# Kernel tuning notes

Hardware: AMD Instinct MI355X
Metric: run time of the kernel (lower is better)

## Reference

```python
import jax, jax.numpy as jnp
import numpy as np

OUTPUT_DIM = 1024  # init kwarg output_dim


def _adaptive_avg_pool_last(x, out_dim):
    """Faithful F.adaptive_avg_pool1d over the last axis (static shapes)."""
    in_dim = x.shape[-1]
    if in_dim % out_dim == 0:
        k = in_dim // out_dim
        return x.reshape(x.shape[:-1] + (out_dim, k)).mean(axis=-1)
    # generic case: window i covers [floor(i*In/Out), ceil((i+1)*In/Out))
    idx = np.arange(out_dim)
    starts = (idx * in_dim) // out_dim
    ends = -((-(idx + 1) * in_dim) // out_dim)
    W = np.zeros((in_dim, out_dim), dtype=np.float32)
    for i in range(out_dim):
        W[starts[i]:ends[i], i] = 1.0 / (ends[i] - starts[i])
    return x @ jnp.asarray(W)


def _per_layer_gram(feat, output_dim):
    N, C, ph, pw = feat.shape
    P = ph * pw
    c_red = min(C, 64)
    f = feat.reshape(N, C, P).transpose(0, 2, 1)        # [N, P, C]
    f = _adaptive_avg_pool_last(f, c_red)               # [N, P, Cr] channel reduction
    fr = f.transpose(0, 2, 1)                           # [N, Cr, P]
    gram = jnp.einsum('ncp,ndp->ncd', fr, fr) / P       # [N, Cr, Cr] per-patch Gram
    return _adaptive_avg_pool_last(gram.reshape(N, c_red * c_red), output_dim)  # [N, output_dim]


def setup_inputs() -> dict:
    key = jax.random.key(0)
    k0, k1 = jax.random.split(key)
    feat0 = jax.random.normal(k0, (6272, 512, 3, 3), dtype=jnp.float32)
    feat1 = jax.random.normal(k1, (6272, 1024, 3, 3), dtype=jnp.float32)
    return {"feat0": feat0, "feat1": feat1}


def reference(feat0, feat1):
    # stack over layers -> [N, L=2, output_dim]
    return jnp.stack(
        [_per_layer_gram(feat0, OUTPUT_DIM), _per_layer_gram(feat1, OUTPUT_DIM)],
        axis=1,
    )
```

## Files before the change

### kernel.cpp

```cpp
#include <hip/hip_runtime.h>


#define N_SAMPLES 6272

template <int CH>
__global__ __launch_bounds__(CH / 4) void patchgram_reg(
    const float* __restrict__ src, float* __restrict__ out)
{
    constexpr int T   = CH / 4;
    constexpr int K   = CH / 64;
    constexpr int TPR = K / 4;
    constexpr float SCALE = 1.0f / (36.0f * (float)(K * K));

    __shared__ float4 fr4[64 * 3];
    __shared__ float4 B4[16 * 3];

    const int n = blockIdx.x;
    const int t = threadIdx.x;

    const float4* __restrict__ g =
        (const float4*)(src + (size_t)n * (CH * 9)) + t * 9;

    float acc[9];
#pragma unroll
    for (int p = 0; p < 9; ++p) acc[p] = 0.f;
#pragma unroll
    for (int j = 0; j < 9; ++j) {
        const float4 v = g[j];
        acc[(4 * j + 0) % 9] += v.x;
        acc[(4 * j + 1) % 9] += v.y;
        acc[(4 * j + 2) % 9] += v.z;
        acc[(4 * j + 3) % 9] += v.w;
    }

#pragma unroll
    for (int p = 0; p < 9; ++p) acc[p] += __shfl_xor(acc[p], 1);
    if (TPR == 4) {
#pragma unroll
        for (int p = 0; p < 9; ++p) acc[p] += __shfl_xor(acc[p], 2);
    }
    if ((t & (TPR - 1)) == 0) {
        const int row = t / TPR;
        fr4[row * 3 + 0] = make_float4(acc[0], acc[1], acc[2], acc[3]);
        fr4[row * 3 + 1] = make_float4(acc[4], acc[5], acc[6], acc[7]);
        fr4[row * 3 + 2] = make_float4(acc[8], 0.f, 0.f, 0.f);
    }
    __syncthreads();

    for (int i = t; i < 144; i += T) {
        const int dg = i / 9;
        const int p  = i - dg * 9;
        const float* fr = (const float*)fr4;
        ((float*)B4)[dg * 12 + p] =
            fr[(4 * dg + 0) * 12 + p] + fr[(4 * dg + 1) * 12 + p] +
            fr[(4 * dg + 2) * 12 + p] + fr[(4 * dg + 3) * 12 + p];
    }
    __syncthreads();

    constexpr int OPT = 1024 / T;
    constexpr int GPR = 16 / OPT;
    const int c     = t / GPR;
    const int dbase = (t % GPR) * OPT;

    const float4 a0 = fr4[c * 3 + 0];
    const float4 a1 = fr4[c * 3 + 1];
    const float4 a2 = fr4[c * 3 + 2];

    float o[OPT];
#pragma unroll
    for (int j = 0; j < OPT; ++j) {
        const int d = dbase + j;
        const float4 b0 = B4[d * 3 + 0];
        const float4 b1 = B4[d * 3 + 1];
        const float4 b2 = B4[d * 3 + 2];
        o[j] = (a0.x * b0.x + a0.y * b0.y + a0.z * b0.z + a0.w * b0.w
              + a1.x * b1.x + a1.y * b1.y + a1.z * b1.z + a1.w * b1.w
              + a2.x * b2.x) * SCALE;
    }

    float* obase = out + (size_t)n * 2048 + c * 16 + dbase;
#pragma unroll
    for (int q = 0; q < OPT / 4; ++q) {
        ((float4*)obase)[q] =
            make_float4(o[4 * q + 0], o[4 * q + 1], o[4 * q + 2], o[4 * q + 3]);
    }
}

extern "C" void kernel_launch(void* const* d_in, const int* in_sizes, int n_in,
                              void* d_out, int out_size, void* d_ws, size_t ws_size,
                              hipStream_t stream) {
    const float* f0 = (const float*)d_in[0];
    const float* f1 = (const float*)d_in[1];
    float* out = (float*)d_out;
    patchgram_reg<512><<<N_SAMPLES, 128, 0, stream>>>(f0, out);
    patchgram_reg<1024><<<N_SAMPLES, 256, 0, stream>>>(f1, out + 1024);
}
```

Measured before the change: 386.3 us.

## Fuse both layer kernels into one launch processing two units per block

```diff
diff --git a/kernel.cpp b/kernel.cpp
--- a/kernel.cpp
+++ b/kernel.cpp
@@ -3,87 +3,142 @@
 
 #define N_SAMPLES 6272
 
-template <int CH>
-__global__ __launch_bounds__(CH / 4) void patchgram_reg(
-    const float* __restrict__ src, float* __restrict__ out)
+constexpr int UNITS0 = N_SAMPLES / 2;
+constexpr int UNITS  = UNITS0 + N_SAMPLES;
+constexpr int GRID   = UNITS / 2;
+
+__global__ __launch_bounds__(256) void patchgram_fused(
+    const float* __restrict__ f0, const float* __restrict__ f1,
+    float* __restrict__ out)
 {
-    constexpr int T   = CH / 4;
-    constexpr int K   = CH / 64;
-    constexpr int TPR = K / 4;
-    constexpr float SCALE = 1.0f / (36.0f * (float)(K * K));
+    __shared__ float4 fr4[2][64 * 3];
+    __shared__ float4 B4[2][16 * 3];
 
-    __shared__ float4 fr4[64 * 3];
-    __shared__ float4 B4[16 * 3];
-
-    const int n = blockIdx.x;
     const int t = threadIdx.x;
 
-    const float4* __restrict__ g =
-        (const float4*)(src + (size_t)n * (CH * 9)) + t * 9;
+    auto unit_ptr = [&](int u) -> const float4* {
+        if (u < UNITS0) {
+            const int s = 2 * u + (t >> 7);
+            return (const float4*)f0 + (size_t)s * 1152 + (size_t)(t & 127) * 9;
+        }
+        const int s = u - UNITS0;
+        return (const float4*)f1 + (size_t)s * 2304 + (size_t)t * 9;
+    };
 
-    float acc[9];
+    auto process = [&](int u, const float4 (&v)[9]) {
+        float acc[9];
 #pragma unroll
-    for (int p = 0; p < 9; ++p) acc[p] = 0.f;
+        for (int p = 0; p < 9; ++p) acc[p] = 0.f;
 #pragma unroll
-    for (int j = 0; j < 9; ++j) {
-        const float4 v = g[j];
-        acc[(4 * j + 0) % 9] += v.x;
-        acc[(4 * j + 1) % 9] += v.y;
-        acc[(4 * j + 2) % 9] += v.z;
-        acc[(4 * j + 3) % 9] += v.w;
-    }
+        for (int j = 0; j < 9; ++j) {
+            acc[(4 * j + 0) % 9] += v[j].x;
+            acc[(4 * j + 1) % 9] += v[j].y;
+            acc[(4 * j + 2) % 9] += v[j].z;
+            acc[(4 * j + 3) % 9] += v[j].w;
+        }
+#pragma unroll
+        for (int p = 0; p < 9; ++p) acc[p] += __shfl_xor(acc[p], 1);
 
+        if (u < UNITS0) {
+            const int half = t >> 7;
+            const int t1   = t & 127;
+            const int s    = 2 * u + half;
+            if ((t1 & 1) == 0) {
+                const int row = t1 >> 1;
+                fr4[half][row * 3 + 0] = make_float4(acc[0], acc[1], acc[2], acc[3]);
+                fr4[half][row * 3 + 1] = make_float4(acc[4], acc[5], acc[6], acc[7]);
+                fr4[half][row * 3 + 2] = make_float4(acc[8], 0.f, 0.f, 0.f);
+            }
+            __syncthreads();
+            {
+                const float* fr = (const float*)fr4[half];
+                float* Bp = (float*)B4[half];
+                int i = t1;
+                int dg = i / 9, p = i - dg * 9;
+                Bp[dg * 12 + p] = fr[(4*dg+0)*12+p] + fr[(4*dg+1)*12+p]
+                                + fr[(4*dg+2)*12+p] + fr[(4*dg+3)*12+p];
+                i = t1 + 128;
+                if (i < 144) {
+                    dg = i / 9; p = i - dg * 9;
+                    Bp[dg * 12 + p] = fr[(4*dg+0)*12+p] + fr[(4*dg+1)*12+p]
+                                    + fr[(4*dg+2)*12+p] + fr[(4*dg+3)*12+p];
+                }
+            }
+            __syncthreads();
+            const int c = t1 >> 1;
+            const int dbase = (t1 & 1) * 8;
+            const float4 a0 = fr4[half][c * 3 + 0];
+            const float4 a1 = fr4[half][c * 3 + 1];
+            const float4 a2 = fr4[half][c * 3 + 2];
+            float o[8];
 #pragma unroll
-    for (int p = 0; p < 9; ++p) acc[p] += __shfl_xor(acc[p], 1);
-    if (TPR == 4) {
+            for (int jj = 0; jj < 8; ++jj) {
+                const int d = dbase + jj;
+                const float4 b0 = B4[half][d * 3 + 0];
+                const float4 b1 = B4[half][d * 3 + 1];
+                const float4 b2 = B4[half][d * 3 + 2];
+                o[jj] = (a0.x*b0.x + a0.y*b0.y + a0.z*b0.z + a0.w*b0.w
+                       + a1.x*b1.x + a1.y*b1.y + a1.z*b1.z + a1.w*b1.w
+                       + a2.x*b2.x) * (1.0f / 2304.0f);
+            }
+            float* ob = out + (size_t)s * 2048 + c * 16 + dbase;
+            ((float4*)ob)[0] = make_float4(o[0], o[1], o[2], o[3]);
+            ((float4*)ob)[1] = make_float4(o[4], o[5], o[6], o[7]);
+            __syncthreads();
+        } else {
+            float acc2[9];
 #pragma unroll
-        for (int p = 0; p < 9; ++p) acc[p] += __shfl_xor(acc[p], 2);
-    }
-    if ((t & (TPR - 1)) == 0) {
-        const int row = t / TPR;
-        fr4[row * 3 + 0] = make_float4(acc[0], acc[1], acc[2], acc[3]);
-        fr4[row * 3 + 1] = make_float4(acc[4], acc[5], acc[6], acc[7]);
-        fr4[row * 3 + 2] = make_float4(acc[8], 0.f, 0.f, 0.f);
-    }
-    __syncthreads();
+            for (int p = 0; p < 9; ++p) acc2[p] = acc[p] + __shfl_xor(acc[p], 2);
+            const int s = u - UNITS0;
+            if ((t & 3) == 0) {
+                const int row = t >> 2;
+                fr4[0][row * 3 + 0] = make_float4(acc2[0], acc2[1], acc2[2], acc2[3]);
+                fr4[0][row * 3 + 1] = make_float4(acc2[4], acc2[5], acc2[6], acc2[7]);
+                fr4[0][row * 3 + 2] = make_float4(acc2[8], 0.f, 0.f, 0.f);
+            }
+            __syncthreads();
+            if (t < 144) {
+                const int dg = t / 9, p = t - dg * 9;
+                const float* fr = (const float*)fr4[0];
+                ((float*)B4[0])[dg*12+p] = fr[(4*dg+0)*12+p] + fr[(4*dg+1)*12+p]
+                                         + fr[(4*dg+2)*12+p] + fr[(4*dg+3)*12+p];
+            }
+            __syncthreads();
+            const int c = t >> 2;
+            const int dbase = (t & 3) * 4;
+            const float4 a0 = fr4[0][c * 3 + 0];
+            const float4 a1 = fr4[0][c * 3 + 1];
+            const float4 a2 = fr4[0][c * 3 + 2];
+            float o[4];
+#pragma unroll
+            for (int jj = 0; jj < 4; ++jj) {
+                const int d = dbase + jj;
+                const float4 b0 = B4[0][d * 3 + 0];
+                const float4 b1 = B4[0][d * 3 + 1];
+                const float4 b2 = B4[0][d * 3 + 2];
+                o[jj] = (a0.x*b0.x + a0.y*b0.y + a0.z*b0.z + a0.w*b0.w
+                       + a1.x*b1.x + a1.y*b1.y + a1.z*b1.z + a1.w*b1.w
+                       + a2.x*b2.x) * (1.0f / 9216.0f);
+            }
+            float* ob = out + (size_t)s * 2048 + 1024 + c * 16 + dbase;
+            *(float4*)ob = make_float4(o[0], o[1], o[2], o[3]);
+            __syncthreads();
+        }
+    };
 
-    for (int i = t; i < 144; i += T) {
-        const int dg = i / 9;
-        const int p  = i - dg * 9;
-        const float* fr = (const float*)fr4;
-        ((float*)B4)[dg * 12 + p] =
-            fr[(4 * dg + 0) * 12 + p] + fr[(4 * dg + 1) * 12 + p] +
-            fr[(4 * dg + 2) * 12 + p] + fr[(4 * dg + 3) * 12 + p];
-    }
-    __syncthreads();
+    const int u0 = blockIdx.x;
+    const int u1 = blockIdx.x + GRID;
 
-    constexpr int OPT = 1024 / T;
-    constexpr int GPR = 16 / OPT;
-    const int c     = t / GPR;
-    const int dbase = (t % GPR) * OPT;
+    float4 v0[9], v1[9];
+    const float4* g0 = unit_ptr(u0);
+#pragma unroll
+    for (int j = 0; j < 9; ++j) v0[j] = g0[j];
+    const float4* g1 = unit_ptr(u1);
+#pragma unroll
+    for (int j = 0; j < 9; ++j) v1[j] = g1[j];
 
-    const float4 a0 = fr4[c * 3 + 0];
-    const float4 a1 = fr4[c * 3 + 1];
-    const float4 a2 = fr4[c * 3 + 2];
-
-    float o[OPT];
-#pragma unroll
-    for (int j = 0; j < OPT; ++j) {
-        const int d = dbase + j;
-        const float4 b0 = B4[d * 3 + 0];
-        const float4 b1 = B4[d * 3 + 1];
-        const float4 b2 = B4[d * 3 + 2];
-        o[j] = (a0.x * b0.x + a0.y * b0.y + a0.z * b0.z + a0.w * b0.w
-              + a1.x * b1.x + a1.y * b1.y + a1.z * b1.z + a1.w * b1.w
-              + a2.x * b2.x) * SCALE;
-    }
-
-    float* obase = out + (size_t)n * 2048 + c * 16 + dbase;
-#pragma unroll
-    for (int q = 0; q < OPT / 4; ++q) {
-        ((float4*)obase)[q] =
-            make_float4(o[4 * q + 0], o[4 * q + 1], o[4 * q + 2], o[4 * q + 3]);
-    }
+    process(u0, v0);
+    process(u1, v1);
 }
 
 extern "C" void kernel_launch(void* const* d_in, const int* in_sizes, int n_in,
@@ -92,6 +147,5 @@
     const float* f0 = (const float*)d_in[0];
     const float* f1 = (const float*)d_in[1];
     float* out = (float*)d_out;
-    patchgram_reg<512><<<N_SAMPLES, 128, 0, stream>>>(f0, out);
-    patchgram_reg<1024><<<N_SAMPLES, 256, 0, stream>>>(f1, out + 1024);
+    patchgram_fused<<<GRID, 256, 0, stream>>>(f0, f1, out);
 }
```

Result: no change. 389.0 us (+0.7%).
